# Performance work log

Hardware: AMD Instinct MI355X
Metric: run time of the kernel (lower is better)

Reference implementation:

```python
import jax, jax.numpy as jnp
import numpy as np


def setup_inputs() -> dict:
    key = jax.random.key(0)
    ks = jax.random.split(key, 6)
    N, E, D = 50000, 400000, 128
    x = jax.random.normal(ks[0], (N, D), dtype=jnp.float32)
    edge_attr = jax.random.normal(ks[1], (E, D), dtype=jnp.float32)
    edge_index = jax.random.randint(ks[2], (2, E), 0, N, dtype=jnp.int64)
    # LatentMLP: two linear layers (3*D -> D -> D) with ReLU activations
    W1 = jax.random.normal(ks[3], (3 * D, D), dtype=jnp.float32) * (1.0 / np.sqrt(3 * D))
    b1 = jnp.zeros((D,), dtype=jnp.float32)
    W2 = jax.random.normal(ks[4], (D, D), dtype=jnp.float32) * (1.0 / np.sqrt(D))
    b2 = jnp.zeros((D,), dtype=jnp.float32)
    return {"x": x, "edge_attr": edge_attr, "edge_index": edge_index,
            "W1": W1, "b1": b1, "W2": W2, "b2": b2}


def reference(x, edge_attr, edge_index, W1, b1, W2, b2):
    src, dst = edge_index[0], edge_index[1]
    # gather node features per edge: [E, D] each
    agg = jnp.concatenate([x[src], x[dst], edge_attr], axis=1)  # [E, 3D]
    h = jax.nn.relu(agg @ W1 + b1)   # [E, D]
    out = jax.nn.relu(h @ W2 + b2)   # [E, D] -> new edge_attr
    return out
```

## Files before the change

### kernel.cpp

```cpp
#include <hip/hip_runtime.h>
#include <hip/hip_bf16.h>

typedef __bf16 bf16_t;
typedef __bf16 bf16x8 __attribute__((ext_vector_type(8)));
typedef __bf16 bf16x4 __attribute__((ext_vector_type(4)));
typedef float  f32x4  __attribute__((ext_vector_type(4)));

#define D 128
#define UV_LDS   131072
#define EDGE_LDS 98304

__device__ __forceinline__ int swz(int r, int c) {
    return (r * D + c) ^ ((r & 7) << 3);
}

__global__ void prep_weights_kernel(const float* __restrict__ W1,
                                    const float* __restrict__ W2,
                                    bf16_t* __restrict__ ws) {
    int t = blockIdx.x * 256 + threadIdx.x;
    int s = t >> 14, r = t & 16383;
    int n = r >> 7, k = r & 127;
    float v = (s < 3) ? W1[(s * 128 + k) * 128 + n] : W2[k * 128 + n];
    ws[t] = (bf16_t)v;
}

__global__ __launch_bounds__(512, 2)
void uv_kernel(const float* __restrict__ x, const bf16_t* __restrict__ ws,
               const float* __restrict__ b1, bf16_t* __restrict__ u,
               bf16_t* __restrict__ v, int N) {
    extern __shared__ __align__(16) bf16_t lds[];
    const int tid = threadIdx.x, lane = tid & 63, wv = tid >> 6;
    const int col0 = lane & 15, krow = lane >> 4, l31 = lane & 31, half = lane >> 5;
    const int gr = lane >> 4, gc = (lane & 15) * 8;
    const int n0 = blockIdx.x * 256 + wv * 32;
    bf16_t* Ach = lds + 32768 + wv * 4096;

    f32x4 xb[16];
#pragma unroll
    for (int j = 0; j < 16; j++) {
        int node = min(n0 + j * 2 + half, N - 1);
        xb[j] = *(const f32x4*)(x + (long long)node * D + l31 * 4);
    }
#pragma unroll
    for (int s = 0; s < 2; s++)
#pragma unroll
        for (int j = 0; j < 4; j++) {
            int row = j * 32 + (tid >> 4), slot = (tid & 15) * 8;
            bf16x8 w = *(const bf16x8*)(ws + s * 16384 + row * 128 + slot);
            *(bf16x8*)&lds[s * 16384 + swz(row, slot)] = w;
        }
    float bias1[8];
#pragma unroll
    for (int n = 0; n < 8; n++) bias1[n] = b1[n * 16 + col0];
#pragma unroll
    for (int j = 0; j < 16; j++) {
        f32x4 vv = xb[j];
        bf16x4 hv = { (bf16_t)vv.x, (bf16_t)vv.y, (bf16_t)vv.z, (bf16_t)vv.w };
        *(bf16x4*)&Ach[swz(j * 2 + half, l31 * 4)] = hv;
    }
    __syncthreads();

    f32x4 aU[2][8], aV[2][8];
#pragma unroll
    for (int m = 0; m < 2; m++)
#pragma unroll
        for (int n = 0; n < 8; n++) { aU[m][n] = (f32x4){0,0,0,0}; aV[m][n] = (f32x4){0,0,0,0}; }
#pragma unroll
    for (int kk = 0; kk < 4; kk++) {
        bf16x8 a0 = *(const bf16x8*)&Ach[swz(col0, kk*32 + krow*8)];
        bf16x8 a1 = *(const bf16x8*)&Ach[swz(16 + col0, kk*32 + krow*8)];
#pragma unroll
        for (int n = 0; n < 8; n++) {
            bf16x8 bU = *(const bf16x8*)&lds[swz(n*16 + col0, kk*32 + krow*8)];
            bf16x8 bV = *(const bf16x8*)&lds[16384 + swz(n*16 + col0, kk*32 + krow*8)];
            aU[0][n] = __builtin_amdgcn_mfma_f32_16x16x32_bf16(a0, bU, aU[0][n], 0,0,0);
            aU[1][n] = __builtin_amdgcn_mfma_f32_16x16x32_bf16(a1, bU, aU[1][n], 0,0,0);
            aV[0][n] = __builtin_amdgcn_mfma_f32_16x16x32_bf16(a0, bV, aV[0][n], 0,0,0);
            aV[1][n] = __builtin_amdgcn_mfma_f32_16x16x32_bf16(a1, bV, aV[1][n], 0,0,0);
        }
    }
#pragma unroll
    for (int m = 0; m < 2; m++)
#pragma unroll
        for (int n = 0; n < 8; n++)
#pragma unroll
            for (int ri = 0; ri < 4; ri++)
                Ach[swz(m*16 + krow*4 + ri, n*16 + col0)] = (bf16_t)(aU[m][n][ri] + bias1[n]);
#pragma unroll
    for (int j = 0; j < 8; j++) {
        int r = j * 4 + gr, node = n0 + r;
        if (node < N) *(bf16x8*)(u + (long long)node * D + gc) = *(const bf16x8*)&Ach[swz(r, gc)];
    }
#pragma unroll
    for (int m = 0; m < 2; m++)
#pragma unroll
        for (int n = 0; n < 8; n++)
#pragma unroll
            for (int ri = 0; ri < 4; ri++)
                Ach[swz(m*16 + krow*4 + ri, n*16 + col0)] = (bf16_t)(aV[m][n][ri]);
#pragma unroll
    for (int j = 0; j < 8; j++) {
        int r = j * 4 + gr, node = n0 + r;
        if (node < N) *(bf16x8*)(v + (long long)node * D + gc) = *(const bf16x8*)&Ach[swz(r, gc)];
    }
}

__global__ __launch_bounds__(512, 1)
void edge_kernel(const bf16_t* __restrict__ u, const bf16_t* __restrict__ v,
                 const float* __restrict__ ea, const int* __restrict__ ei,
                 const bf16_t* __restrict__ ws, const float* __restrict__ b2,
                 float* __restrict__ out, int E) {
    extern __shared__ __align__(16) bf16_t lds[];
    const int tid = threadIdx.x, lane = tid & 63, wv = tid >> 6;
    const int col0 = lane & 15, krow = lane >> 4, l31 = lane & 31, half = lane >> 5;
    const int gr = lane >> 4, gc = (lane & 15) * 8;
    bf16_t* Ach = lds + 32768 + wv * 2048;

    const int totg = (E + 15) >> 4;
    const int gstr = gridDim.x * 8;
    int g = blockIdx.x * 8 + wv;

    f32x4  eaR[8];
    bf16x8 uR[4], vR[4];
    int sidxN = 0, didxN = 0;

    if (g < totg) {
        int er = min(g * 16 + col0, E - 1);
        int sidx = ei[er], didx = ei[E + er];
#pragma unroll
        for (int j = 0; j < 8; j++) {
            int e = min(g * 16 + j * 2 + half, E - 1);
            eaR[j] = *(const f32x4*)(ea + (long long)e * D + l31 * 4);
        }
#pragma unroll
        for (int j = 0; j < 4; j++) { int gi = __shfl(sidx, j * 4 + gr); uR[j] = *(const bf16x8*)(u + (long long)gi * D + gc); }
#pragma unroll
        for (int j = 0; j < 4; j++) { int gi = __shfl(didx, j * 4 + gr); vR[j] = *(const bf16x8*)(v + (long long)gi * D + gc); }
        int gn = g + gstr;
        if (gn < totg) {
            int er2 = min(gn * 16 + col0, E - 1);
            sidxN = ei[er2]; didxN = ei[E + er2];
        }
    }
#pragma unroll
    for (int s = 0; s < 2; s++)
#pragma unroll
        for (int j = 0; j < 4; j++) {
            int row = j * 32 + (tid >> 4), slot = (tid & 15) * 8;
            bf16x8 w = *(const bf16x8*)(ws + (2 + s) * 16384 + row * 128 + slot);
            *(bf16x8*)&lds[s * 16384 + swz(row, slot)] = w;
        }
    float bias2[8];
#pragma unroll
    for (int n = 0; n < 8; n++) bias2[n] = b2[n * 16 + col0];
    __syncthreads();

    while (g < totg) {
        const int gn = g + gstr;

#pragma unroll
        for (int j = 0; j < 8; j++) {
            f32x4 vv = eaR[j];
            bf16x4 hv = { (bf16_t)vv.x, (bf16_t)vv.y, (bf16_t)vv.z, (bf16_t)vv.w };
            *(bf16x4*)&Ach[swz(j * 2 + half, l31 * 4)] = hv;
        }
        if (gn < totg) {
#pragma unroll
            for (int j = 0; j < 8; j++) {
                int e = min(gn * 16 + j * 2 + half, E - 1);
                eaR[j] = *(const f32x4*)(ea + (long long)e * D + l31 * 4);
            }
        }
        int sidx2 = 0, didx2 = 0;
        int g2 = gn + gstr;
        if (g2 < totg) {
            int er = min(g2 * 16 + col0, E - 1);
            sidx2 = ei[er]; didx2 = ei[E + er];
        }

        f32x4 acc[8];
#pragma unroll
        for (int n = 0; n < 8; n++) acc[n] = (f32x4){0,0,0,0};
#pragma unroll
        for (int kk = 0; kk < 4; kk++) {
            bf16x8 a = *(const bf16x8*)&Ach[swz(col0, kk*32 + krow*8)];
#pragma unroll
            for (int n = 0; n < 8; n++) {
                bf16x8 b = *(const bf16x8*)&lds[swz(n*16 + col0, kk*32 + krow*8)];
                acc[n] = __builtin_amdgcn_mfma_f32_16x16x32_bf16(a, b, acc[n], 0, 0, 0);
            }
        }

#pragma unroll
        for (int j = 0; j < 4; j++) {
            bf16x8 su = uR[j], sv = vR[j], sr;
#pragma unroll
            for (int t = 0; t < 8; t++) sr[t] = (bf16_t)((float)su[t] + (float)sv[t]);
            *(bf16x8*)&Ach[swz(j * 4 + gr, gc)] = sr;
        }
        if (gn < totg) {
#pragma unroll
            for (int j = 0; j < 4; j++) { int gi = __shfl(sidxN, j * 4 + gr); uR[j] = *(const bf16x8*)(u + (long long)gi * D + gc); }
#pragma unroll
            for (int j = 0; j < 4; j++) { int gi = __shfl(didxN, j * 4 + gr); vR[j] = *(const bf16x8*)(v + (long long)gi * D + gc); }
        }

#pragma unroll
        for (int n = 0; n < 8; n++)
#pragma unroll
            for (int ri = 0; ri < 4; ri++) {
                int row = krow * 4 + ri, col = n * 16 + col0;
                float sval = (float)Ach[swz(row, col)];
                float hv = fmaxf(acc[n][ri] + sval, 0.f);
                Ach[swz(row, col)] = (bf16_t)hv;
            }

#pragma unroll
        for (int n = 0; n < 8; n++) acc[n] = (f32x4){0,0,0,0};
#pragma unroll
        for (int kk = 0; kk < 4; kk++) {
            bf16x8 a = *(const bf16x8*)&Ach[swz(col0, kk*32 + krow*8)];
#pragma unroll
            for (int n = 0; n < 8; n++) {
                bf16x8 b = *(const bf16x8*)&lds[16384 + swz(n*16 + col0, kk*32 + krow*8)];
                acc[n] = __builtin_amdgcn_mfma_f32_16x16x32_bf16(a, b, acc[n], 0, 0, 0);
            }
        }

#pragma unroll
        for (int n = 0; n < 8; n++)
#pragma unroll
            for (int ri = 0; ri < 4; ri++) {
                int e = g * 16 + krow * 4 + ri;
                if (e < E) out[(long long)e * D + n*16 + col0] = fmaxf(acc[n][ri] + bias2[n], 0.f);
            }

        g = gn; sidxN = sidx2; didxN = didx2;
    }
}

extern "C" void kernel_launch(void* const* d_in, const int* in_sizes, int n_in,
                              void* d_out, int out_size, void* d_ws, size_t ws_size,
                              hipStream_t stream) {
    const float* x  = (const float*)d_in[0];
    const float* ea = (const float*)d_in[1];
    const int*   ei = (const int*)d_in[2];
    const float* W1 = (const float*)d_in[3];
    const float* b1 = (const float*)d_in[4];
    const float* W2 = (const float*)d_in[5];
    const float* b2 = (const float*)d_in[6];
    float* out = (float*)d_out;

    const int E = in_sizes[1] / D;
    const int N = in_sizes[0] / D;

    bf16_t* wsl = (bf16_t*)d_ws;
    bf16_t* uu  = wsl + 4 * 16384;
    bf16_t* vv  = uu + (size_t)N * D;

    prep_weights_kernel<<<256, 256, 0, stream>>>(W1, W2, wsl);

    hipFuncSetAttribute(reinterpret_cast<const void*>(uv_kernel),
                        hipFuncAttributeMaxDynamicSharedMemorySize, UV_LDS);
    hipFuncSetAttribute(reinterpret_cast<const void*>(edge_kernel),
                        hipFuncAttributeMaxDynamicSharedMemorySize, EDGE_LDS);

    uv_kernel<<<(N + 255) / 256, 512, UV_LDS, stream>>>(x, wsl, b1, uu, vv, N);

    edge_kernel<<<256, 512, EDGE_LDS, stream>>>(uu, vv, ea, ei, wsl, b2, out, E);
}
```

Measured before the change: 135.5 us.

## Process 32 edges per wave to reuse weight fragments across two MFMA rows

Each wave now handles a 32-edge tile instead of 16. Every B-fragment read from LDS feeds two MFMAs, which halves the LDS weight traffic per edge. The first-layer epilogue is also restructured: the accumulator is written to LDS and then combined with the gathered u+v rows using vectorized reads, replacing the per-element read-modify-write. In exchange, register use (ea, u, v prefetch buffers and accumulators) and per-wave LDS roughly double, and the grid stride covers fewer groups per block, which may hurt occupancy or load balance.

```diff
diff --git a/kernel.cpp b/kernel.cpp
--- a/kernel.cpp
+++ b/kernel.cpp
@@ -8,7 +8,7 @@
 
 #define D 128
 #define UV_LDS   131072
-#define EDGE_LDS 98304
+#define EDGE_LDS 131072
 
 __device__ __forceinline__ int swz(int r, int c) {
     return (r * D + c) ^ ((r & 7) << 3);
@@ -114,31 +114,31 @@
     const int tid = threadIdx.x, lane = tid & 63, wv = tid >> 6;
     const int col0 = lane & 15, krow = lane >> 4, l31 = lane & 31, half = lane >> 5;
     const int gr = lane >> 4, gc = (lane & 15) * 8;
-    bf16_t* Ach = lds + 32768 + wv * 2048;
-
-    const int totg = (E + 15) >> 4;
+    bf16_t* Ach = lds + 32768 + wv * 4096;
+
+    const int totg = (E + 31) >> 5;
     const int gstr = gridDim.x * 8;
     int g = blockIdx.x * 8 + wv;
 
-    f32x4  eaR[8];
-    bf16x8 uR[4], vR[4];
+    f32x4  eaR[16];
+    bf16x8 uR[8], vR[8];
     int sidxN = 0, didxN = 0;
 
     if (g < totg) {
-        int er = min(g * 16 + col0, E - 1);
+        int er = min(g * 32 + l31, E - 1);
         int sidx = ei[er], didx = ei[E + er];
 #pragma unroll
-        for (int j = 0; j < 8; j++) {
-            int e = min(g * 16 + j * 2 + half, E - 1);
+        for (int j = 0; j < 16; j++) {
+            int e = min(g * 32 + j * 2 + half, E - 1);
             eaR[j] = *(const f32x4*)(ea + (long long)e * D + l31 * 4);
         }
 #pragma unroll
-        for (int j = 0; j < 4; j++) { int gi = __shfl(sidx, j * 4 + gr); uR[j] = *(const bf16x8*)(u + (long long)gi * D + gc); }
-#pragma unroll
-        for (int j = 0; j < 4; j++) { int gi = __shfl(didx, j * 4 + gr); vR[j] = *(const bf16x8*)(v + (long long)gi * D + gc); }
+        for (int j = 0; j < 8; j++) { int gi = __shfl(sidx, j * 4 + gr); uR[j] = *(const bf16x8*)(u + (long long)gi * D + gc); }
+#pragma unroll
+        for (int j = 0; j < 8; j++) { int gi = __shfl(didx, j * 4 + gr); vR[j] = *(const bf16x8*)(v + (long long)gi * D + gc); }
         int gn = g + gstr;
         if (gn < totg) {
-            int er2 = min(gn * 16 + col0, E - 1);
+            int er2 = min(gn * 32 + l31, E - 1);
             sidxN = ei[er2]; didxN = ei[E + er2];
         }
     }
@@ -159,81 +159,92 @@
         const int gn = g + gstr;
 
 #pragma unroll
-        for (int j = 0; j < 8; j++) {
+        for (int j = 0; j < 16; j++) {
             f32x4 vv = eaR[j];
             bf16x4 hv = { (bf16_t)vv.x, (bf16_t)vv.y, (bf16_t)vv.z, (bf16_t)vv.w };
             *(bf16x4*)&Ach[swz(j * 2 + half, l31 * 4)] = hv;
         }
         if (gn < totg) {
 #pragma unroll
-            for (int j = 0; j < 8; j++) {
-                int e = min(gn * 16 + j * 2 + half, E - 1);
+            for (int j = 0; j < 16; j++) {
+                int e = min(gn * 32 + j * 2 + half, E - 1);
                 eaR[j] = *(const f32x4*)(ea + (long long)e * D + l31 * 4);
             }
         }
         int sidx2 = 0, didx2 = 0;
         int g2 = gn + gstr;
         if (g2 < totg) {
-            int er = min(g2 * 16 + col0, E - 1);
+            int er = min(g2 * 32 + l31, E - 1);
             sidx2 = ei[er]; didx2 = ei[E + er];
         }
 
-        f32x4 acc[8];
-#pragma unroll
-        for (int n = 0; n < 8; n++) acc[n] = (f32x4){0,0,0,0};
+        f32x4 acc[2][8];
+#pragma unroll
+        for (int m = 0; m < 2; m++)
+#pragma unroll
+            for (int n = 0; n < 8; n++) acc[m][n] = (f32x4){0,0,0,0};
 #pragma unroll
         for (int kk = 0; kk < 4; kk++) {
-            bf16x8 a = *(const bf16x8*)&Ach[swz(col0, kk*32 + krow*8)];
+            bf16x8 a0 = *(const bf16x8*)&Ach[swz(     col0, kk*32 + krow*8)];
+            bf16x8 a1 = *(const bf16x8*)&Ach[swz(16 + col0, kk*32 + krow*8)];
 #pragma unroll
             for (int n = 0; n < 8; n++) {
                 bf16x8 b = *(const bf16x8*)&lds[swz(n*16 + col0, kk*32 + krow*8)];
-                acc[n] = __builtin_amdgcn_mfma_f32_16x16x32_bf16(a, b, acc[n], 0, 0, 0);
+                acc[0][n] = __builtin_amdgcn_mfma_f32_16x16x32_bf16(a0, b, acc[0][n], 0, 0, 0);
+                acc[1][n] = __builtin_amdgcn_mfma_f32_16x16x32_bf16(a1, b, acc[1][n], 0, 0, 0);
             }
         }
 
 #pragma unroll
-        for (int j = 0; j < 4; j++) {
-            bf16x8 su = uR[j], sv = vR[j], sr;
-#pragma unroll
-            for (int t = 0; t < 8; t++) sr[t] = (bf16_t)((float)su[t] + (float)sv[t]);
-            *(bf16x8*)&Ach[swz(j * 4 + gr, gc)] = sr;
-        }
+        for (int m = 0; m < 2; m++)
+#pragma unroll
+            for (int n = 0; n < 8; n++)
+#pragma unroll
+                for (int ri = 0; ri < 4; ri++)
+                    Ach[swz(m*16 + krow*4 + ri, n*16 + col0)] = (bf16_t)acc[m][n][ri];
+
+#pragma unroll
+        for (int j = 0; j < 8; j++) {
+            bf16x8 p8 = *(const bf16x8*)&Ach[swz(j * 4 + gr, gc)];
+            bf16x8 su = uR[j], sv = vR[j], h8;
+#pragma unroll
+            for (int t = 0; t < 8; t++)
+                h8[t] = (bf16_t)fmaxf((float)p8[t] + (float)su[t] + (float)sv[t], 0.f);
+            *(bf16x8*)&Ach[swz(j * 4 + gr, gc)] = h8;
+        }
+
         if (gn < totg) {
 #pragma unroll
-            for (int j = 0; j < 4; j++) { int gi = __shfl(sidxN, j * 4 + gr); uR[j] = *(const bf16x8*)(u + (long long)gi * D + gc); }
-#pragma unroll
-            for (int j = 0; j < 4; j++) { int gi = __shfl(didxN, j * 4 + gr); vR[j] = *(const bf16x8*)(v + (long long)gi * D + gc); }
-        }
-
-#pragma unroll
-        for (int n = 0; n < 8; n++)
-#pragma unroll
-            for (int ri = 0; ri < 4; ri++) {
-                int row = krow * 4 + ri, col = n * 16 + col0;
-                float sval = (float)Ach[swz(row, col)];
-                float hv = fmaxf(acc[n][ri] + sval, 0.f);
-                Ach[swz(row, col)] = (bf16_t)hv;
-            }
-
-#pragma unroll
-        for (int n = 0; n < 8; n++) acc[n] = (f32x4){0,0,0,0};
+            for (int j = 0; j < 8; j++) { int gi = __shfl(sidxN, j * 4 + gr); uR[j] = *(const bf16x8*)(u + (long long)gi * D + gc); }
+#pragma unroll
+            for (int j = 0; j < 8; j++) { int gi = __shfl(didxN, j * 4 + gr); vR[j] = *(const bf16x8*)(v + (long long)gi * D + gc); }
+        }
+
+#pragma unroll
+        for (int m = 0; m < 2; m++)
+#pragma unroll
+            for (int n = 0; n < 8; n++) acc[m][n] = (f32x4){0,0,0,0};
 #pragma unroll
         for (int kk = 0; kk < 4; kk++) {
-            bf16x8 a = *(const bf16x8*)&Ach[swz(col0, kk*32 + krow*8)];
+            bf16x8 a0 = *(const bf16x8*)&Ach[swz(     col0, kk*32 + krow*8)];
+            bf16x8 a1 = *(const bf16x8*)&Ach[swz(16 + col0, kk*32 + krow*8)];
 #pragma unroll
             for (int n = 0; n < 8; n++) {
                 bf16x8 b = *(const bf16x8*)&lds[16384 + swz(n*16 + col0, kk*32 + krow*8)];
-                acc[n] = __builtin_amdgcn_mfma_f32_16x16x32_bf16(a, b, acc[n], 0, 0, 0);
+                acc[0][n] = __builtin_amdgcn_mfma_f32_16x16x32_bf16(a0, b, acc[0][n], 0, 0, 0);
+                acc[1][n] = __builtin_amdgcn_mfma_f32_16x16x32_bf16(a1, b, acc[1][n], 0, 0, 0);
             }
         }
 
 #pragma unroll
-        for (int n = 0; n < 8; n++)
-#pragma unroll
-            for (int ri = 0; ri < 4; ri++) {
-                int e = g * 16 + krow * 4 + ri;
-                if (e < E) out[(long long)e * D + n*16 + col0] = fmaxf(acc[n][ri] + bias2[n], 0.f);
-            }
+        for (int m = 0; m < 2; m++)
+#pragma unroll
+            for (int n = 0; n < 8; n++)
+#pragma unroll
+                for (int ri = 0; ri < 4; ri++) {
+                    int e = g * 32 + m*16 + krow * 4 + ri;
+                    if (e < E) out[(long long)e * D + n*16 + col0] = fmaxf(acc[m][n][ri] + bias2[n], 0.f);
+                }
 
         g = gn; sidxN = sidx2; didxN = didx2;
     }
```

New measurement: 394.1 us. 191% more time.
